# Performance work log

Measured on AMD Instinct MI355X. Metric: run time of the kernel, lower is better.

Reference implementation:

```python
import jax, jax.numpy as jnp
import numpy as np

N = 10000        # total_node
IN_SIZE = 128
OUT_SIZE = 128


def setup_inputs() -> dict:
    key = jax.random.key(0)
    k_adj, k_x, k_wn, k_ws = jax.random.split(key, 4)
    adj = jax.random.uniform(k_adj, (N, N), dtype=jnp.float32)           # package[1]
    old_node_embedding = jax.random.normal(k_x, (N, IN_SIZE), dtype=jnp.float32)
    # nn.Linear weights are stored [out, in]
    W_nei = jax.random.normal(k_wn, (OUT_SIZE, IN_SIZE), dtype=jnp.float32) * (1.0 / np.sqrt(IN_SIZE))
    W_self = jax.random.normal(k_ws, (OUT_SIZE, IN_SIZE), dtype=jnp.float32) * (1.0 / np.sqrt(IN_SIZE))
    return {
        "adj": adj,
        "old_node_embedding": old_node_embedding,
        "W_nei": W_nei,
        "W_self": W_self,
        "out_size": OUT_SIZE,
        "use_divce": 0,
    }


def reference(adj, old_node_embedding, W_nei, W_self, out_size, use_divce):
    # Vectorized form of the per-node torch loop:
    #   nei_gather[n]   = adj[n, :] @ X                (torch.mm per node)
    #   nei_info[n]     = nei_gather[n] @ W_nei^T      (nei_update1)
    #   self_info[n]    = X[n] @ W_self^T              (self_node_update1)
    #   new_emb[n]      = act(nei_info[n] + self_info[n])
    # active_method fixed to tanh.
    nei_gather = adj @ old_node_embedding                         # [N, in]
    nei_info = nei_gather @ W_nei.T                               # [N, out]
    self_info = old_node_embedding @ W_self.T                     # [N, out]
    return jnp.tanh(nei_info + self_info)
```

## Files before the change

### kernel.cpp

```cpp
#include <hip/hip_runtime.h>
#include <cmath>


#define N_NODES 10000
#define EMB 128
#define XNT_STRIDE 10240
#define KC 832
#define NKCH 13

typedef __bf16 bf16x8 __attribute__((ext_vector_type(8)));
typedef float  f32x4  __attribute__((ext_vector_type(4)));

#define GLOAD_LDS16(gp, lp)                                                  \
    __builtin_amdgcn_global_load_lds(                                        \
        (const __attribute__((address_space(1))) void*)(gp),                 \
        (__attribute__((address_space(3))) void*)(lp), 16, 0, 0)

__device__ __forceinline__ void split8(const float4& x0, const float4& x1,
                                       bf16x8& h, bf16x8& l) {
    float f[8] = {x0.x, x0.y, x0.z, x0.w, x1.x, x1.y, x1.z, x1.w};
#pragma unroll
    for (int i = 0; i < 8; ++i) {
        __bf16 hh = (__bf16)f[i];
        h[i] = hh;
        l[i] = (__bf16)(f[i] - (float)hh);
    }
}

__global__ __launch_bounds__(256) void prep_kernel(
    const float* __restrict__ X, const float* __restrict__ Wn,
    __bf16* __restrict__ xnt_hi, __bf16* __restrict__ xnt_lo)
{
    __shared__ float Xl[32 * EMB];
    const int tid = threadIdx.x;
    const int n0 = blockIdx.x * 32;

    if (blockIdx.x == 0) {
        bf16x8 z;
#pragma unroll
        for (int i = 0; i < 8; ++i) z[i] = (__bf16)0.0f;
        for (int g = tid; g < 128 * 30; g += 256) {
            int col = g / 30, j = g % 30;
            size_t off = (size_t)col * XNT_STRIDE + N_NODES + j * 8;
            *(bf16x8*)(xnt_hi + off) = z;
            *(bf16x8*)(xnt_lo + off) = z;
        }
    }

#pragma unroll
    for (int i = 0; i < 4; ++i) {
        int idx = tid + i * 256;
        int r = idx >> 5;
        int c4 = (idx & 31) << 2;
        int row = n0 + r;
        float4 v = make_float4(0.f, 0.f, 0.f, 0.f);
        if (row < N_NODES) v = *(const float4*)(X + (size_t)row * EMB + c4);
        *(float4*)(Xl + r * EMB + c4) = v;
    }
    __syncthreads();

    const int c = tid & 127;
    const int half = tid >> 7;
    const float* wrow = Wn + c * EMB;

    float acc[16];
#pragma unroll
    for (int r = 0; r < 16; ++r) acc[r] = 0.f;

    for (int k4 = 0; k4 < 32; ++k4) {
        float4 w = *(const float4*)(wrow + k4 * 4);
#pragma unroll
        for (int r = 0; r < 16; ++r) {
            float4 x = *(const float4*)(Xl + (half * 16 + r) * EMB + k4 * 4);
            acc[r] += x.x * w.x + x.y * w.y + x.z * w.z + x.w * w.w;
        }
    }

    if (n0 + half * 16 < N_NODES) {
        bf16x8 h0, h1, l0, l1;
#pragma unroll
        for (int r = 0; r < 16; ++r) {
            float f = acc[r];
            __bf16 h = (__bf16)f;
            __bf16 l = (__bf16)(f - (float)h);
            if (r < 8) { h0[r] = h; l0[r] = l; }
            else       { h1[r - 8] = h; l1[r - 8] = l; }
        }
        size_t base = (size_t)c * XNT_STRIDE + n0 + half * 16;
        *(bf16x8*)(xnt_hi + base)     = h0;
        *(bf16x8*)(xnt_hi + base + 8) = h1;
        *(bf16x8*)(xnt_lo + base)     = l0;
        *(bf16x8*)(xnt_lo + base + 8) = l1;
    }
}

__global__ __launch_bounds__(256, 2) void gemm_kernel(
    const float* __restrict__ adj, const __bf16* __restrict__ xnt_hi,
    const __bf16* __restrict__ xnt_lo, float* __restrict__ Ppart)
{
    __shared__ float  Af [2][128 * 32];
    __shared__ __bf16 Bhs[2][128 * 32];
    __shared__ __bf16 Bls[2][128 * 32];

    const int tid = threadIdx.x;
    const int m0 = blockIdx.x * 128;
    const int kc0 = blockIdx.y * KC;
    const int kc_end = min(kc0 + KC, N_NODES);
    const int nsub = (kc_end - kc0 + 31) >> 5;

    const int lane = tid & 63;
    const int wave = tid >> 6;
    const int wm = (wave & 1) * 64;
    const int wn = (wave >> 1) * 64;
    const int fr = lane & 15;
    const int q  = lane >> 4;
    const int f7 = fr & 7;

    const int a_c4 = ((tid & 7) ^ ((tid >> 3) & 7)) * 4;
    size_t a_rowoff[4];
#pragma unroll
    for (int i = 0; i < 4; ++i) {
        int r = i * 32 + (tid >> 3);
        if (m0 + r >= N_NODES) r &= 15;
        a_rowoff[i] = (size_t)(m0 + r) * N_NODES;
    }
    const int b_k8 = ((tid & 3) ^ ((tid >> 3) & 3)) * 8;
    size_t b_coloff[2];
#pragma unroll
    for (int i = 0; i < 2; ++i)
        b_coloff[i] = (size_t)(i * 64 + (tid >> 2)) * XNT_STRIDE;

    f32x4 acc[4][4];
#pragma unroll
    for (int mt = 0; mt < 4; ++mt)
#pragma unroll
        for (int nt = 0; nt < 4; ++nt)
#pragma unroll
            for (int e = 0; e < 4; ++e) acc[mt][nt][e] = 0.f;

    auto stage = [&](int ks, int pb) {
        const int k0 = kc0 + ks * 32;
#pragma unroll
        for (int i = 0; i < 4; ++i) {
            int kk = k0 + a_c4;
            if (kk + 4 > kc_end) kk = kc0;
            GLOAD_LDS16(adj + a_rowoff[i] + kk, &Af[pb][(i * 256 + tid) * 4]);
        }
#pragma unroll
        for (int i = 0; i < 2; ++i) {
            GLOAD_LDS16(xnt_hi + b_coloff[i] + k0 + b_k8,
                        &Bhs[pb][(i * 256 + tid) * 8]);
            GLOAD_LDS16(xnt_lo + b_coloff[i] + k0 + b_k8,
                        &Bls[pb][(i * 256 + tid) * 8]);
        }
    };

    stage(0, 0);
    __syncthreads();

    for (int ks = 0; ks < nsub; ++ks) {
        const int cb = ks & 1;
        if (ks + 1 < nsub) stage(ks + 1, cb ^ 1);

        const float*  af  = &Af [cb][0];
        const __bf16* bhp = &Bhs[cb][0];
        const __bf16* blp = &Bls[cb][0];

        bf16x8 ah[4], al[4], bh[4], bl[4];
#pragma unroll
        for (int mt = 0; mt < 4; ++mt) {
            int r = wm + mt * 16 + fr;
            int c0 = q * 2;
            int pc0 = c0 ^ f7;
            int pc1 = (c0 + 1) ^ f7;
            float4 fa = *(const float4*)(af + r * 32 + pc0 * 4);
            float4 fb = *(const float4*)(af + r * 32 + pc1 * 4);
            split8(fa, fb, ah[mt], al[mt]);
        }
#pragma unroll
        for (int nt = 0; nt < 4; ++nt) {
            int col = wn + nt * 16 + fr;
            int pq = q ^ ((fr >> 1) & 3);
            bh[nt] = *(const bf16x8*)(bhp + col * 32 + pq * 8);
            bl[nt] = *(const bf16x8*)(blp + col * 32 + pq * 8);
        }
#pragma unroll
        for (int mt = 0; mt < 4; ++mt)
#pragma unroll
            for (int nt = 0; nt < 4; ++nt) {
                acc[mt][nt] = __builtin_amdgcn_mfma_f32_16x16x32_bf16(ah[mt], bh[nt], acc[mt][nt], 0, 0, 0);
                acc[mt][nt] = __builtin_amdgcn_mfma_f32_16x16x32_bf16(ah[mt], bl[nt], acc[mt][nt], 0, 0, 0);
                acc[mt][nt] = __builtin_amdgcn_mfma_f32_16x16x32_bf16(al[mt], bh[nt], acc[mt][nt], 0, 0, 0);
            }

        __syncthreads();
    }

    float* P = Ppart + (size_t)blockIdx.y * ((size_t)N_NODES * EMB);
#pragma unroll
    for (int mt = 0; mt < 4; ++mt) {
        int rbase = m0 + wm + mt * 16 + q * 4;
#pragma unroll
        for (int nt = 0; nt < 4; ++nt) {
            int col = wn + nt * 16 + fr;
#pragma unroll
            for (int r = 0; r < 4; ++r) {
                int row = rbase + r;
                if (row < N_NODES)
                    P[(size_t)row * EMB + col] = acc[mt][nt][r];
            }
        }
    }
}

__global__ __launch_bounds__(256) void epi_kernel(
    const float* __restrict__ X, const float* __restrict__ Wself,
    const float* __restrict__ Ppart, float* __restrict__ out)
{
    __shared__ float Xl[32 * EMB];
    const int tid = threadIdx.x;
    const int n0 = blockIdx.x * 32;

#pragma unroll
    for (int i = 0; i < 4; ++i) {
        int idx = tid + i * 256;
        int r = idx >> 5;
        int c4 = (idx & 31) << 2;
        int row = n0 + r;
        float4 v = make_float4(0.f, 0.f, 0.f, 0.f);
        if (row < N_NODES) v = *(const float4*)(X + (size_t)row * EMB + c4);
        *(float4*)(Xl + r * EMB + c4) = v;
    }
    __syncthreads();

    const int c = tid & 127;
    const int half = tid >> 7;
    const float* wrow = Wself + c * EMB;

    float acc[16];
#pragma unroll
    for (int r = 0; r < 16; ++r) acc[r] = 0.f;

    for (int k4 = 0; k4 < 32; ++k4) {
        float4 w = *(const float4*)(wrow + k4 * 4);
#pragma unroll
        for (int r = 0; r < 16; ++r) {
            float4 x = *(const float4*)(Xl + (half * 16 + r) * EMB + k4 * 4);
            acc[r] += x.x * w.x + x.y * w.y + x.z * w.z + x.w * w.w;
        }
    }

    if (n0 + half * 16 < N_NODES) {
        const size_t rb = (size_t)(n0 + half * 16) * EMB + c;
#pragma unroll
        for (int p = 0; p < NKCH; ++p) {
            const float* Pp = Ppart + (size_t)p * ((size_t)N_NODES * EMB) + rb;
#pragma unroll
            for (int r = 0; r < 16; ++r)
                acc[r] += Pp[(size_t)r * EMB];
        }
#pragma unroll
        for (int r = 0; r < 16; ++r)
            out[rb + (size_t)r * EMB] = tanhf(acc[r]);
    }
}

__global__ __launch_bounds__(256) void gemm0_kernel(
    const float* __restrict__ adj, const float* __restrict__ X,
    float* __restrict__ Y)
{
    __shared__ float As[128 * 33];
    __shared__ float Xs[32 * 132];
    const int tid = threadIdx.x;
    const int m0 = blockIdx.x * 128;
    const int kc0 = blockIdx.y * KC;
    const int kc_end = min(kc0 + KC, N_NODES);
    const int nsub = (kc_end - kc0 + 31) >> 5;

    const int am = tid >> 1, akq = tid & 1;
    const bool arv = (m0 + am) < N_NODES;
    const float* arow_p = adj + (size_t)(m0 + am) * N_NODES;
    const int xr = tid >> 3, xq = tid & 7;
    const int mq = tid >> 4, nq = tid & 15;

    float acc[8][8];
#pragma unroll
    for (int i = 0; i < 8; ++i)
#pragma unroll
        for (int j = 0; j < 8; ++j) acc[i][j] = 0.f;

    for (int ks = 0; ks < nsub; ++ks) {
        int k0 = kc0 + ks * 32;
#pragma unroll
        for (int i = 0; i < 4; ++i) {
            int k = k0 + akq * 16 + i * 4;
            float4 v = make_float4(0.f, 0.f, 0.f, 0.f);
            if (arv && k < kc_end) v = *(const float4*)(arow_p + k);
            float* d = As + am * 33 + akq * 16 + i * 4;
            d[0] = v.x; d[1] = v.y; d[2] = v.z; d[3] = v.w;
        }
#pragma unroll
        for (int i = 0; i < 4; ++i) {
            int c0 = xq * 16 + i * 4;
            int krow = k0 + xr;
            float4 v = make_float4(0.f, 0.f, 0.f, 0.f);
            if (krow < kc_end) v = *(const float4*)(X + (size_t)krow * EMB + c0);
            *(float4*)(Xs + xr * 132 + c0) = v;
        }
        __syncthreads();
        for (int k = 0; k < 32; ++k) {
            float a8[8];
#pragma unroll
            for (int i = 0; i < 8; ++i) a8[i] = As[(mq * 8 + i) * 33 + k];
            float4 x0 = *(const float4*)(Xs + k * 132 + nq * 8);
            float4 x1 = *(const float4*)(Xs + k * 132 + nq * 8 + 4);
            float x8[8] = { x0.x, x0.y, x0.z, x0.w, x1.x, x1.y, x1.z, x1.w };
#pragma unroll
            for (int i = 0; i < 8; ++i)
#pragma unroll
                for (int j = 0; j < 8; ++j) acc[i][j] += a8[i] * x8[j];
        }
        __syncthreads();
    }
#pragma unroll
    for (int i = 0; i < 8; ++i) {
        int row = m0 + mq * 8 + i;
        if (row < N_NODES) {
#pragma unroll
            for (int j = 0; j < 8; ++j)
                atomicAdd(Y + (size_t)row * EMB + nq * 8 + j, acc[i][j]);
        }
    }
}

__global__ __launch_bounds__(256) void epi0_kernel(
    const float* __restrict__ X, const float* __restrict__ Wn,
    const float* __restrict__ Ws, float* __restrict__ out)
{
    __shared__ float Xl[32 * EMB];
    __shared__ float Yl[32 * EMB];
    const int tid = threadIdx.x;
    const int n0 = blockIdx.x * 32;

#pragma unroll
    for (int i = 0; i < 4; ++i) {
        int idx = tid + i * 256;
        int r = idx >> 5;
        int c4 = (idx & 31) << 2;
        int row = n0 + r;
        float4 vx = make_float4(0.f, 0.f, 0.f, 0.f);
        float4 vy = vx;
        if (row < N_NODES) {
            vx = *(const float4*)(X + (size_t)row * EMB + c4);
            vy = *(const float4*)(out + (size_t)row * EMB + c4);
        }
        *(float4*)(Xl + r * EMB + c4) = vx;
        *(float4*)(Yl + r * EMB + c4) = vy;
    }
    __syncthreads();

    const int c = tid & 127;
    const int half = tid >> 7;
    const float* wn = Wn + c * EMB;
    const float* ws = Ws + c * EMB;

    float accn[16], accs[16];
#pragma unroll
    for (int r = 0; r < 16; ++r) { accn[r] = 0.f; accs[r] = 0.f; }

    for (int k4 = 0; k4 < 32; ++k4) {
        float4 a = *(const float4*)(wn + k4 * 4);
        float4 b = *(const float4*)(ws + k4 * 4);
#pragma unroll
        for (int r = 0; r < 16; ++r) {
            float4 y = *(const float4*)(Yl + (half * 16 + r) * EMB + k4 * 4);
            float4 x = *(const float4*)(Xl + (half * 16 + r) * EMB + k4 * 4);
            accn[r] += y.x * a.x + y.y * a.y + y.z * a.z + y.w * a.w;
            accs[r] += x.x * b.x + x.y * b.y + x.z * b.z + x.w * b.w;
        }
    }
#pragma unroll
    for (int r = 0; r < 16; ++r) {
        int row = n0 + half * 16 + r;
        if (row < N_NODES)
            out[(size_t)row * EMB + c] = tanhf(accn[r] + accs[r]);
    }
}

extern "C" void kernel_launch(void* const* d_in, const int* in_sizes, int n_in,
                              void* d_out, int out_size, void* d_ws, size_t ws_size,
                              hipStream_t stream) {
    const float* adj = (const float*)d_in[0];
    const float* X   = (const float*)d_in[1];
    const float* Wn  = (const float*)d_in[2];
    const float* Ws  = (const float*)d_in[3];
    float* out = (float*)d_out;

    const size_t xnt_elems = (size_t)EMB * XNT_STRIDE;
    const size_t xnt_bytes = xnt_elems * 2 * sizeof(unsigned short);
    const size_t part_bytes = (size_t)NKCH * N_NODES * EMB * sizeof(float);

    if (ws_size >= xnt_bytes + part_bytes) {
        __bf16* xh = (__bf16*)d_ws;
        __bf16* xl = xh + xnt_elems;
        float* Ppart = (float*)((char*)d_ws + xnt_bytes);
        prep_kernel<<<(N_NODES + 31) / 32, 256, 0, stream>>>(X, Wn, xh, xl);
        gemm_kernel<<<dim3((N_NODES + 127) / 128, NKCH), 256, 0, stream>>>(adj, xh, xl, Ppart);
        epi_kernel<<<(N_NODES + 31) / 32, 256, 0, stream>>>(X, Ws, Ppart, out);
    } else {
        hipMemsetAsync(d_out, 0, (size_t)N_NODES * EMB * sizeof(float), stream);
        gemm0_kernel<<<dim3((N_NODES + 127) / 128, NKCH), 256, 0, stream>>>(adj, X, out);
        epi0_kernel<<<(N_NODES + 31) / 32, 256, 0, stream>>>(X, Wn, Ws, out);
    }
}
```

Measured before the change: 604.7 us.

## Halve GEMM M-tile and read B fragments directly from global memory

The adjacency GEMM tile shrinks from 128 to 64 rows, and the LDS staging of the bf16 hi/lo X^T operand is removed. Each wave now loads its B fragments straight from global memory (expected to hit in L2) every k-step. This cuts LDS use and register pressure so four blocks per CU fit, and doubles the grid for better latency hiding on the bandwidth-bound fp32 adj stream. The cost is that B fragments are re-fetched per block and per wave, and the global B loads sit on the critical path without prefetch, which may stall the MFMAs.

```diff
diff --git a/kernel.cpp b/kernel.cpp
--- a/kernel.cpp
+++ b/kernel.cpp
@@ -94,45 +94,47 @@
     }
 }
 
-__global__ __launch_bounds__(256, 2) void gemm_kernel(
+__global__ __launch_bounds__(256, 4) void gemm_kernel(
     const float* __restrict__ adj, const __bf16* __restrict__ xnt_hi,
     const __bf16* __restrict__ xnt_lo, float* __restrict__ Ppart)
 {
-    __shared__ float  Af [2][128 * 32];
-    __shared__ __bf16 Bhs[2][128 * 32];
-    __shared__ __bf16 Bls[2][128 * 32];
+    __shared__ float Af[2][64 * 32];
 
     const int tid = threadIdx.x;
-    const int m0 = blockIdx.x * 128;
+    const int m0 = blockIdx.x * 64;
     const int kc0 = blockIdx.y * KC;
     const int kc_end = min(kc0 + KC, N_NODES);
     const int nsub = (kc_end - kc0 + 31) >> 5;
 
     const int lane = tid & 63;
     const int wave = tid >> 6;
-    const int wm = (wave & 1) * 64;
+    const int wm = (wave & 1) * 32;
     const int wn = (wave >> 1) * 64;
     const int fr = lane & 15;
     const int q  = lane >> 4;
     const int f7 = fr & 7;
 
     const int a_c4 = ((tid & 7) ^ ((tid >> 3) & 7)) * 4;
-    size_t a_rowoff[4];
-#pragma unroll
-    for (int i = 0; i < 4; ++i) {
+    size_t a_rowoff[2];
+#pragma unroll
+    for (int i = 0; i < 2; ++i) {
         int r = i * 32 + (tid >> 3);
         if (m0 + r >= N_NODES) r &= 15;
         a_rowoff[i] = (size_t)(m0 + r) * N_NODES;
     }
-    const int b_k8 = ((tid & 3) ^ ((tid >> 3) & 3)) * 8;
-    size_t b_coloff[2];
-#pragma unroll
-    for (int i = 0; i < 2; ++i)
-        b_coloff[i] = (size_t)(i * 64 + (tid >> 2)) * XNT_STRIDE;
-
-    f32x4 acc[4][4];
-#pragma unroll
-    for (int mt = 0; mt < 4; ++mt)
+
+    const __bf16* bhp[4];
+    const __bf16* blp[4];
+#pragma unroll
+    for (int nt = 0; nt < 4; ++nt) {
+        int col = wn + nt * 16 + fr;
+        bhp[nt] = xnt_hi + (size_t)col * XNT_STRIDE;
+        blp[nt] = xnt_lo + (size_t)col * XNT_STRIDE;
+    }
+
+    f32x4 acc[2][4];
+#pragma unroll
+    for (int mt = 0; mt < 2; ++mt)
 #pragma unroll
         for (int nt = 0; nt < 4; ++nt)
 #pragma unroll
@@ -141,18 +143,11 @@
     auto stage = [&](int ks, int pb) {
         const int k0 = kc0 + ks * 32;
 #pragma unroll
-        for (int i = 0; i < 4; ++i) {
+        for (int i = 0; i < 2; ++i) {
             int kk = k0 + a_c4;
             if (kk + 4 > kc_end) kk = kc0;
             GLOAD_LDS16(adj + a_rowoff[i] + kk, &Af[pb][(i * 256 + tid) * 4]);
         }
-#pragma unroll
-        for (int i = 0; i < 2; ++i) {
-            GLOAD_LDS16(xnt_hi + b_coloff[i] + k0 + b_k8,
-                        &Bhs[pb][(i * 256 + tid) * 8]);
-            GLOAD_LDS16(xnt_lo + b_coloff[i] + k0 + b_k8,
-                        &Bls[pb][(i * 256 + tid) * 8]);
-        }
     };
 
     stage(0, 0);
@@ -162,13 +157,19 @@
         const int cb = ks & 1;
         if (ks + 1 < nsub) stage(ks + 1, cb ^ 1);
 
-        const float*  af  = &Af [cb][0];
-        const __bf16* bhp = &Bhs[cb][0];
-        const __bf16* blp = &Bls[cb][0];
-
-        bf16x8 ah[4], al[4], bh[4], bl[4];
-#pragma unroll
-        for (int mt = 0; mt < 4; ++mt) {
+        const int kq = kc0 + ks * 32 + q * 8;
+
+        bf16x8 bh[4], bl[4];
+#pragma unroll
+        for (int nt = 0; nt < 4; ++nt) {
+            bh[nt] = *(const bf16x8*)(bhp[nt] + kq);
+            bl[nt] = *(const bf16x8*)(blp[nt] + kq);
+        }
+
+        const float* af = &Af[cb][0];
+        bf16x8 ah[2], al[2];
+#pragma unroll
+        for (int mt = 0; mt < 2; ++mt) {
             int r = wm + mt * 16 + fr;
             int c0 = q * 2;
             int pc0 = c0 ^ f7;
@@ -177,15 +178,9 @@
             float4 fb = *(const float4*)(af + r * 32 + pc1 * 4);
             split8(fa, fb, ah[mt], al[mt]);
         }
-#pragma unroll
-        for (int nt = 0; nt < 4; ++nt) {
-            int col = wn + nt * 16 + fr;
-            int pq = q ^ ((fr >> 1) & 3);
-            bh[nt] = *(const bf16x8*)(bhp + col * 32 + pq * 8);
-            bl[nt] = *(const bf16x8*)(blp + col * 32 + pq * 8);
-        }
-#pragma unroll
-        for (int mt = 0; mt < 4; ++mt)
+
+#pragma unroll
+        for (int mt = 0; mt < 2; ++mt)
 #pragma unroll
             for (int nt = 0; nt < 4; ++nt) {
                 acc[mt][nt] = __builtin_amdgcn_mfma_f32_16x16x32_bf16(ah[mt], bh[nt], acc[mt][nt], 0, 0, 0);
@@ -198,7 +193,7 @@
 
     float* P = Ppart + (size_t)blockIdx.y * ((size_t)N_NODES * EMB);
 #pragma unroll
-    for (int mt = 0; mt < 4; ++mt) {
+    for (int mt = 0; mt < 2; ++mt) {
         int rbase = m0 + wm + mt * 16 + q * 4;
 #pragma unroll
         for (int nt = 0; nt < 4; ++nt) {
@@ -405,7 +400,7 @@
         __bf16* xl = xh + xnt_elems;
         float* Ppart = (float*)((char*)d_ws + xnt_bytes);
         prep_kernel<<<(N_NODES + 31) / 32, 256, 0, stream>>>(X, Wn, xh, xl);
-        gemm_kernel<<<dim3((N_NODES + 127) / 128, NKCH), 256, 0, stream>>>(adj, xh, xl, Ppart);
+        gemm_kernel<<<dim3((N_NODES + 63) / 64, NKCH), 256, 0, stream>>>(adj, xh, xl, Ppart);
         epi_kernel<<<(N_NODES + 31) / 32, 256, 0, stream>>>(X, Ws, Ppart, out);
     } else {
         hipMemsetAsync(d_out, 0, (size_t)N_NODES * EMB * sizeof(float), stream);
```

Result: slower. 755.7 us (+25.0%).
